# Performance work log

Hardware: AMD Instinct MI355X
Metric: run time of the kernel (lower is better)

The kernel has to match this reference:

```python
import jax, jax.numpy as jnp
import numpy as np

NUM_HEADS = 12
LN_EPS = 1e-5


def _pe(seq_len, d_model):
    # sinusoidal positional encoding buffer (constant)
    pos = np.arange(seq_len, dtype=np.float32)[:, None]
    div = np.exp(np.arange(0, d_model, 2, dtype=np.float32) * (-np.log(10000.0) / d_model))
    pe = np.zeros((seq_len, d_model), dtype=np.float32)
    pe[:, 0::2] = np.sin(pos * div)
    pe[:, 1::2] = np.cos(pos * div)
    return jnp.asarray(pe)


def _ln(x, g, b):
    m = jnp.mean(x, axis=-1, keepdims=True)
    v = jnp.mean(jnp.square(x - m), axis=-1, keepdims=True)
    return (x - m) * jax.lax.rsqrt(v + LN_EPS) * g + b


def setup_inputs() -> dict:
    key = jax.random.key(0)
    B, S, V, D, L, F = 8, 512, 32000, 768, 4, 3072
    ks = jax.random.split(key, 8)
    sc = 0.02
    return {
        "x_ids": jax.random.randint(ks[0], (B, S), 0, V),
        "emb": jax.random.normal(ks[1], (V, D), jnp.float32) * sc,
        "Wq": jax.random.normal(ks[2], (L, D, D), jnp.float32) * sc,
        "bq": jnp.zeros((L, D), jnp.float32),
        "Wk": jax.random.normal(ks[3], (L, D, D), jnp.float32) * sc,
        "bk": jnp.zeros((L, D), jnp.float32),
        "Wv": jax.random.normal(ks[4], (L, D, D), jnp.float32) * sc,
        "bv": jnp.zeros((L, D), jnp.float32),
        "Wo": jax.random.normal(ks[5], (L, D, D), jnp.float32) * sc,
        "bo": jnp.zeros((L, D), jnp.float32),
        "g1": jnp.ones((L, D), jnp.float32),
        "bn1": jnp.zeros((L, D), jnp.float32),
        "W1": jax.random.normal(ks[6], (L, D, F), jnp.float32) * sc,
        "bw1": jnp.zeros((L, F), jnp.float32),
        "W2": jax.random.normal(ks[7], (L, F, D), jnp.float32) * sc,
        "bw2": jnp.zeros((L, D), jnp.float32),
        "g2": jnp.ones((L, D), jnp.float32),
        "bn2": jnp.zeros((L, D), jnp.float32),
    }


def reference(x_ids, emb, Wq, bq, Wk, bk, Wv, bv, Wo, bo, g1, bn1, W1, bw1, W2, bw2, g2, bn2):
    B, S = x_ids.shape
    D = emb.shape[1]
    H = NUM_HEADS
    dk = D // H
    h = emb[x_ids] + _pe(S, D)  # [B,S,D]; dropout is identity (eval)

    def layer(h, p):
        wq, bq_, wk, bk_, wv, bv_, wo, bo_, g1_, bn1_, w1, b1_, w2, b2_, g2_, bn2_ = p

        def heads(y):  # [B,S,D] -> [B,H,S,dk]
            return y.reshape(B, S, H, dk).transpose(0, 2, 1, 3)

        q = heads(h @ wq + bq_)
        k = heads(h @ wk + bk_)
        v = heads(h @ wv + bv_)
        scores = jnp.einsum('bhqd,bhkd->bhqk', q, k) / jnp.sqrt(jnp.float32(dk))
        attn = jax.nn.softmax(scores, axis=-1)
        o = jnp.einsum('bhqk,bhkd->bhqd', attn, v)
        o = o.transpose(0, 2, 1, 3).reshape(B, S, D)
        h = _ln(h + o @ wo + bo_, g1_, bn1_)
        ff = jax.nn.relu(h @ w1 + b1_) @ w2 + b2_
        h = _ln(h + ff, g2_, bn2_)
        return h, None

    h, _ = jax.lax.scan(layer, h, (Wq, bq, Wk, bk, Wv, bv, Wo, bo, g1, bn1, W1, bw1, W2, bw2, g2, bn2))
    return h
```

## Files before the change

kernel.cpp:

```cpp
#include <hip/hip_runtime.h>
#include <stdint.h>

#define B_ 8
#define S_ 512
#define D_ 768
#define H_ 12
#define DK_ 64
#define F_ 3072
#define L_ 4
#define NT_ (B_*S_)
#define BH_ (B_*H_)
#define DQKV_ 2304

typedef __bf16 bf16x8 __attribute__((ext_vector_type(8)));
typedef float f32x4 __attribute__((ext_vector_type(4)));
typedef unsigned short u16x8 __attribute__((ext_vector_type(8)));

static __device__ __forceinline__ unsigned short f2b(float f){
  union { float f; unsigned u; } x; x.f = f;
  unsigned r = x.u + 0x7fffu + ((x.u >> 16) & 1u);
  return (unsigned short)(r >> 16);
}

static __device__ __forceinline__ void gload16(const void* g, void* l){
  __builtin_amdgcn_global_load_lds((const __attribute__((address_space(1))) void*)g,
                                   (__attribute__((address_space(3))) void*)l, 16, 0, 0);
}

static __device__ __forceinline__ float wsum(float v){
  #pragma unroll
  for (int off = 32; off; off >>= 1) v += __shfl_xor(v, off);
  return v;
}

__global__ void wconv_kernel(const float* __restrict__ in, unsigned short* __restrict__ out,
                             int Rr, int Cc, size_t outLS, int rowBase){
  __shared__ float tile[32][33];
  const int l = blockIdx.z;
  in  += (size_t)l*Rr*Cc;
  out += (size_t)l*outLS;
  const int c0 = blockIdx.x*32, r0 = blockIdx.y*32;
  const int tx = threadIdx.x, ty = threadIdx.y;
  #pragma unroll
  for (int i = 0; i < 4; ++i)
    tile[ty+8*i][tx] = in[(size_t)(r0+ty+8*i)*Cc + c0+tx];
  __syncthreads();
  #pragma unroll
  for (int i = 0; i < 4; ++i)
    out[(size_t)(rowBase + c0+ty+8*i)*Rr + r0+tx] = f2b(tile[tx][ty+8*i]);
}

__global__ void bcat_kernel(const float* __restrict__ bq, const float* __restrict__ bk,
                            const float* __restrict__ bv, float* __restrict__ out){
  int i = blockIdx.x*256 + threadIdx.x;
  if (i >= L_*DQKV_) return;
  int l = i / DQKV_, c = i % DQKV_;
  float v = (c < D_) ? bq[l*D_ + c] : (c < 2*D_) ? bk[l*D_ + c - D_] : bv[l*D_ + c - 2*D_];
  out[i] = v;
}

__global__ __launch_bounds__(256) void pe_kernel(float* __restrict__ pe){
  int u = blockIdx.x*256 + threadIdx.x;
  if (u >= S_*384) return;
  int dp = u % 384, s = u / 384;
  int d0 = dp*2;
  float div = __expf((float)d0 * (-9.210340371976184f / 768.0f));
  float ang = (float)s * div;
  pe[(size_t)s*D_ + d0]     = sinf(ang);
  pe[(size_t)s*D_ + d0 + 1] = cosf(ang);
}

__global__ __launch_bounds__(256) void embed_kernel(const int* __restrict__ ids,
                                                    const float* __restrict__ emb,
                                                    const float* __restrict__ pe,
                                                    float* __restrict__ h,
                                                    unsigned short* __restrict__ hb){
  int u = blockIdx.x*256 + threadIdx.x;
  if (u >= NT_*192) return;
  int c = u % 192, t = u / 192, s = t % S_;
  int id = ids[t];
  float4 e = reinterpret_cast<const float4*>(emb + (size_t)id*D_)[c];
  float4 p = reinterpret_cast<const float4*>(pe  + (size_t)s*D_)[c];
  float4 r; r.x = e.x+p.x; r.y = e.y+p.y; r.z = e.z+p.z; r.w = e.w+p.w;
  reinterpret_cast<float4*>(h + (size_t)t*D_)[c] = r;
  ushort4 ub; ub.x = f2b(r.x); ub.y = f2b(r.y); ub.z = f2b(r.z); ub.w = f2b(r.w);
  reinterpret_cast<ushort4*>(hb + (size_t)t*D_)[c] = ub;
}

template<int TN, int KS, bool BIAS, bool RES, bool RELU, bool OUTB>
__global__ __launch_bounds__(256)
void gemm_kernel(const unsigned short* __restrict__ A,
                 const unsigned short* __restrict__ Bt,
                 const float* __restrict__ bias,
                 const float* __restrict__ resid,
                 void* __restrict__ outp,
                 int M, int N, int K)
{
  constexpr int WN = TN/2;
  constexpr int JF = WN/16;
  constexpr int SLOTS = (128+TN)/64;
  __shared__ __attribute__((aligned(16))) unsigned short As[3][128*32];
  __shared__ __attribute__((aligned(16))) unsigned short Bs[3][TN*32];
  const int tid = threadIdx.x;
  const int w = tid >> 6, l = tid & 63;
  const int wm = w >> 1, wn = w & 1;
  const int c16 = l & 15, g = l >> 4;

  const int nwg = gridDim.x;
  const int cpx = nwg >> 3;
  const int sw  = (blockIdx.x & 7)*cpx + (blockIdx.x >> 3);
  const int nbx = N/TN;
  const int nby = M/128;
  const int bx = sw % nbx;
  const int t2 = sw / nbx;
  const int by = t2 % nby;
  const int ks = t2 / nby;
  const int bm = by*128, bn = bx*TN;
  const int Klen = K / KS;
  const int kBeg = ks*Klen;
  const int nk = Klen >> 5;

  auto stage = [&](int buf, int k0){
    #pragma unroll
    for (int s = 0; s < SLOTS; ++s) {
      const int base = s*4096 + w*1024;
      const int x    = base + l*16;
      if (s < 2) {
        const int row  = x >> 6;
        const int csrc = ((x >> 4) & 3) ^ ((row >> 2) & 3);
        gload16(A + (size_t)(bm+row)*K + k0 + csrc*8, (void*)(As[buf] + base/2));
      } else {
        const int o2   = x - 8192;
        const int row  = o2 >> 6;
        const int csrc = ((o2 >> 4) & 3) ^ ((row >> 2) & 3);
        gload16(Bt + (size_t)(bn+row)*K + k0 + csrc*8, (void*)(Bs[buf] + (base-8192)/2));
      }
    }
  };

  f32x4 acc[4][JF] = {};
  const int cswz = (g ^ (c16 >> 2)) * 8;

  stage(0, kBeg);
  stage(1, kBeg + 32);
  stage(2, kBeg + 64);

  for (int t = 0; t < nk; ++t) {
    const int cur = t % 3;
    const int rem = nk - 1 - t;
    if constexpr (SLOTS == 4) {
      if (rem >= 2)      asm volatile("s_waitcnt vmcnt(8)" ::: "memory");
      else if (rem == 1) asm volatile("s_waitcnt vmcnt(4)" ::: "memory");
      else               asm volatile("s_waitcnt vmcnt(0)" ::: "memory");
    } else {
      if (rem >= 2)      asm volatile("s_waitcnt vmcnt(6)" ::: "memory");
      else if (rem == 1) asm volatile("s_waitcnt vmcnt(3)" ::: "memory");
      else               asm volatile("s_waitcnt vmcnt(0)" ::: "memory");
    }
    __builtin_amdgcn_s_barrier();
    __builtin_amdgcn_sched_barrier(0);

    bf16x8 af[4], bfr[JF];
    #pragma unroll
    for (int i = 0; i < 4; ++i)
      af[i]  = *reinterpret_cast<const bf16x8*>(&As[cur][(wm*64 + i*16 + c16)*32 + cswz]);
    #pragma unroll
    for (int j = 0; j < JF; ++j)
      bfr[j] = *reinterpret_cast<const bf16x8*>(&Bs[cur][(wn*WN + j*16 + c16)*32 + cswz]);
    asm volatile("s_waitcnt lgkmcnt(0)" ::: "memory");
    __builtin_amdgcn_sched_barrier(0);
    __builtin_amdgcn_s_barrier();

    if (t + 3 < nk) stage(cur, kBeg + (t+3)*32);

    __builtin_amdgcn_s_setprio(1);
    #pragma unroll
    for (int i = 0; i < 4; ++i)
      #pragma unroll
      for (int j = 0; j < JF; ++j)
        acc[i][j] = __builtin_amdgcn_mfma_f32_16x16x32_bf16(af[i], bfr[j], acc[i][j], 0, 0, 0);
    __builtin_amdgcn_s_setprio(0);
  }

  float* outF = (float*)outp + (size_t)ks*M*N;
  unsigned short* outB = (unsigned short*)outp;
  #pragma unroll
  for (int i = 0; i < 4; ++i) {
    #pragma unroll
    for (int e = 0; e < 4; ++e) {
      const int row = bm + wm*64 + i*16 + (l>>4)*4 + e;
      #pragma unroll
      for (int j = 0; j < JF; ++j) {
        const int col = bn + wn*WN + j*16 + (l&15);
        float v = acc[i][j][e];
        if constexpr (BIAS) v += bias[col];
        if constexpr (RES)  v += resid[(size_t)row*N + col];
        if constexpr (RELU) v = fmaxf(v, 0.f);
        if constexpr (OUTB) outB[(size_t)row*N + col] = f2b(v);
        else                outF[(size_t)row*N + col] = v;
      }
    }
  }
}

__global__ void vtrans_kernel(const unsigned short* __restrict__ v,
                              unsigned short* __restrict__ vt, int ld){
  __shared__ unsigned short tile[32][33];
  const int z = blockIdx.z; const int b = z / H_, hh = z % H_;
  const int j0 = blockIdx.x*32;
  const int d0 = blockIdx.y*32;
  const int tx = threadIdx.x, ty = threadIdx.y;
  const unsigned short* src = v + (size_t)b*S_*ld + hh*DK_;
  #pragma unroll
  for (int i = 0; i < 4; ++i)
    tile[ty+8*i][tx] = src[(size_t)(j0+ty+8*i)*ld + d0+tx];
  __syncthreads();
  unsigned short* dst = vt + (size_t)z*DK_*S_;
  #pragma unroll
  for (int i = 0; i < 4; ++i)
    dst[(size_t)(d0+ty+8*i)*S_ + j0+tx] = tile[tx][ty+8*i];
}

__global__ __launch_bounds__(256)
void fattn_kernel(const unsigned short* __restrict__ qkv,
                  const unsigned short* __restrict__ vt,
                  unsigned short* __restrict__ o)
{
  __shared__ __attribute__((aligned(16))) unsigned short Plds[4*4096];
  const int tid = threadIdx.x;
  const int w = tid >> 6, l = tid & 63;
  const int g = l >> 4, c16 = l & 15;
  const int z = blockIdx.y; const int b = z / H_, hh = z % H_;
  const int q0 = blockIdx.x*128 + w*32;

  const unsigned short* qp = qkv + (size_t)b*S_*DQKV_ + hh*DK_;
  const unsigned short* kp = qp + D_;
  const unsigned short* vv = vt + (size_t)z*DK_*S_;
  char* pbase = (char*)Plds + w*8192;

  bf16x8 qf[2][2];
  #pragma unroll
  for (int jf = 0; jf < 2; ++jf)
    #pragma unroll
    for (int kc = 0; kc < 2; ++kc)
      qf[jf][kc] = *reinterpret_cast<const bf16x8*>(qp + (size_t)(q0 + jf*16 + c16)*DQKV_ + kc*32 + g*8);

  f32x4 acc_o[2][4] = {};
  float m_run[2] = {-1e30f, -1e30f};
  float l_run[2] = {0.f, 0.f};

  for (int kb = 0; kb < S_/128; ++kb) {
    f32x4 acc_s[8][2] = {};
    #pragma unroll
    for (int kt = 0; kt < 8; ++kt) {
      bf16x8 af0 = *reinterpret_cast<const bf16x8*>(kp + (size_t)(kb*128 + kt*16 + c16)*DQKV_ + 0*32 + g*8);
      bf16x8 af1 = *reinterpret_cast<const bf16x8*>(kp + (size_t)(kb*128 + kt*16 + c16)*DQKV_ + 1*32 + g*8);
      #pragma unroll
      for (int jf = 0; jf < 2; ++jf) {
        acc_s[kt][jf] = __builtin_amdgcn_mfma_f32_16x16x32_bf16(af0, qf[jf][0], acc_s[kt][jf], 0, 0, 0);
        acc_s[kt][jf] = __builtin_amdgcn_mfma_f32_16x16x32_bf16(af1, qf[jf][1], acc_s[kt][jf], 0, 0, 0);
      }
    }
    float fac[2];
    #pragma unroll
    for (int jf = 0; jf < 2; ++jf) {
      float vmax = -1e30f;
      #pragma unroll
      for (int kt = 0; kt < 8; ++kt)
        #pragma unroll
        for (int e = 0; e < 4; ++e) {
          acc_s[kt][jf][e] *= 0.125f;
          vmax = fmaxf(vmax, acc_s[kt][jf][e]);
        }
      vmax = fmaxf(vmax, __shfl_xor(vmax, 16));
      vmax = fmaxf(vmax, __shfl_xor(vmax, 32));
      const float m_new = fmaxf(m_run[jf], vmax);
      fac[jf] = __expf(m_run[jf] - m_new);
      float ps = 0.f;
      #pragma unroll
      for (int kt = 0; kt < 8; ++kt)
        #pragma unroll
        for (int e = 0; e < 4; ++e) {
          float p = __expf(acc_s[kt][jf][e] - m_new);
          acc_s[kt][jf][e] = p;
          ps += p;
        }
      ps += __shfl_xor(ps, 16);
      ps += __shfl_xor(ps, 32);
      l_run[jf] = l_run[jf]*fac[jf] + ps;
      m_run[jf] = m_new;
      const int q = jf*16 + c16;
      #pragma unroll
      for (int kt = 0; kt < 8; ++kt) {
        uint2 val;
        val.x = (unsigned)f2b(acc_s[kt][jf][0]) | ((unsigned)f2b(acc_s[kt][jf][1]) << 16);
        val.y = (unsigned)f2b(acc_s[kt][jf][2]) | ((unsigned)f2b(acc_s[kt][jf][3]) << 16);
        int off = (q*256 + kt*32 + g*8) ^ ((q & 7) << 4);
        *reinterpret_cast<uint2*>(pbase + off) = val;
      }
    }
    #pragma unroll
    for (int jr = 0; jr < 2; ++jr)
      #pragma unroll
      for (int e = 0; e < 4; ++e) {
        const float fr = __shfl(fac[jr], g*4 + e);
        #pragma unroll
        for (int jd = 0; jd < 4; ++jd)
          acc_o[jr][jd][e] *= fr;
      }
    #pragma unroll
    for (int kc = 0; kc < 4; ++kc) {
      bf16x8 pa[2], vfr[4];
      #pragma unroll
      for (int jf = 0; jf < 2; ++jf) {
        const int q = jf*16 + c16;
        int off = (q*256 + kc*64 + g*16) ^ ((q & 7) << 4);
        pa[jf] = *reinterpret_cast<const bf16x8*>(pbase + off);
      }
      #pragma unroll
      for (int jd = 0; jd < 4; ++jd)
        vfr[jd] = *reinterpret_cast<const bf16x8*>(vv + (size_t)(jd*16 + c16)*S_ + kb*128 + kc*32 + g*8);
      #pragma unroll
      for (int jf = 0; jf < 2; ++jf)
        #pragma unroll
        for (int jd = 0; jd < 4; ++jd)
          acc_o[jf][jd] = __builtin_amdgcn_mfma_f32_16x16x32_bf16(pa[jf], vfr[jd], acc_o[jf][jd], 0, 0, 0);
    }
  }

  float invl[2] = {1.f/l_run[0], 1.f/l_run[1]};
  unsigned short* ob = o + (size_t)b*S_*D_ + hh*DK_;
  #pragma unroll
  for (int jr = 0; jr < 2; ++jr)
    #pragma unroll
    for (int e = 0; e < 4; ++e) {
      const float ir = __shfl(invl[jr], g*4 + e);
      const int r = q0 + jr*16 + g*4 + e;
      #pragma unroll
      for (int jd = 0; jd < 4; ++jd)
        ob[(size_t)r*D_ + jd*16 + c16] = f2b(acc_o[jr][jd][e] * ir);
    }
}

template<int NP, bool EXTRA>
__global__ __launch_bounds__(256)
void ln_kernel(const float* __restrict__ x,
               const float* __restrict__ resid, const float* __restrict__ bias2,
               const float* __restrict__ g, const float* __restrict__ bta,
               float* __restrict__ ho, unsigned short* __restrict__ hb)
{
  const int w = threadIdx.x >> 6, l = threadIdx.x & 63;
  const size_t row = (size_t)blockIdx.x*4 + w;
  float4 vx[3]; float s1 = 0.f, s2 = 0.f;
  #pragma unroll
  for (int c = 0; c < 3; ++c) {
    vx[c] = reinterpret_cast<const float4*>(x + row*D_)[l + 64*c];
    #pragma unroll
    for (int p = 1; p < NP; ++p) {
      float4 a = reinterpret_cast<const float4*>(x + (size_t)p*NT_*D_ + row*D_)[l + 64*c];
      vx[c].x += a.x; vx[c].y += a.y; vx[c].z += a.z; vx[c].w += a.w;
    }
    if constexpr (EXTRA) {
      float4 r  = reinterpret_cast<const float4*>(resid + row*D_)[l + 64*c];
      float4 bb = reinterpret_cast<const float4*>(bias2)[l + 64*c];
      vx[c].x += r.x + bb.x; vx[c].y += r.y + bb.y;
      vx[c].z += r.z + bb.z; vx[c].w += r.w + bb.w;
    }
    s1 += vx[c].x + vx[c].y + vx[c].z + vx[c].w;
    s2 += vx[c].x*vx[c].x + vx[c].y*vx[c].y + vx[c].z*vx[c].z + vx[c].w*vx[c].w;
  }
  s1 = wsum(s1); s2 = wsum(s2);
  const float mean = s1 * (1.f/768.f);
  const float var  = s2 * (1.f/768.f) - mean*mean;
  const float rs   = rsqrtf(var + 1e-5f);
  const float4* gp = reinterpret_cast<const float4*>(g);
  const float4* bp = reinterpret_cast<const float4*>(bta);
  float4* hp = reinterpret_cast<float4*>(ho + row*D_);
  #pragma unroll
  for (int c = 0; c < 3; ++c) {
    float4 gg = gp[l + 64*c], bb = bp[l + 64*c];
    float4 r;
    r.x = (vx[c].x - mean)*rs*gg.x + bb.x;
    r.y = (vx[c].y - mean)*rs*gg.y + bb.y;
    r.z = (vx[c].z - mean)*rs*gg.z + bb.z;
    r.w = (vx[c].w - mean)*rs*gg.w + bb.w;
    hp[l + 64*c] = r;
    ushort4 u; u.x = f2b(r.x); u.y = f2b(r.y); u.z = f2b(r.z); u.w = f2b(r.w);
    *reinterpret_cast<ushort4*>(hb + row*D_ + (size_t)(l + 64*c)*4) = u;
  }
}

extern "C" void kernel_launch(void* const* d_in, const int* in_sizes, int n_in,
                              void* d_out, int out_size, void* d_ws, size_t ws_size,
                              hipStream_t stream)
{
  const int*   x_ids = (const int*)  d_in[0];
  const float* emb   = (const float*)d_in[1];
  const float* Wq    = (const float*)d_in[2];
  const float* bq    = (const float*)d_in[3];
  const float* Wk    = (const float*)d_in[4];
  const float* bk    = (const float*)d_in[5];
  const float* Wv    = (const float*)d_in[6];
  const float* bv    = (const float*)d_in[7];
  const float* Wo    = (const float*)d_in[8];
  const float* bo    = (const float*)d_in[9];
  const float* g1    = (const float*)d_in[10];
  const float* bn1   = (const float*)d_in[11];
  const float* W1    = (const float*)d_in[12];
  const float* bw1   = (const float*)d_in[13];
  const float* W2    = (const float*)d_in[14];
  const float* bw2   = (const float*)d_in[15];
  const float* g2    = (const float*)d_in[16];
  const float* bn2   = (const float*)d_in[17];

  char* ws = (char*)d_ws;
  size_t off = 0;
  auto alloc = [&](size_t bytes) -> void* {
    void* p = ws + off; off += (bytes + 255) & ~((size_t)255); return p;
  };
  unsigned short* WqkvT = (unsigned short*)alloc((size_t)L_*DQKV_*D_*2);
  unsigned short* WoT = (unsigned short*)alloc((size_t)L_*D_*D_*2);
  unsigned short* W1T = (unsigned short*)alloc((size_t)L_*D_*F_*2);
  unsigned short* W2T = (unsigned short*)alloc((size_t)L_*D_*F_*2);
  float*          bqkv= (float*)         alloc((size_t)L_*DQKV_*4);
  float*          pe  = (float*)         alloc((size_t)S_*D_*4);
  float*          h   = (float*)         alloc((size_t)NT_*D_*4);
  unsigned short* hb  = (unsigned short*)alloc((size_t)NT_*D_*2);
  unsigned short* qkv = (unsigned short*)alloc((size_t)NT_*DQKV_*2);
  unsigned short* vt  = (unsigned short*)alloc((size_t)BH_*DK_*S_*2);
  unsigned short* attnb = (unsigned short*)alloc((size_t)NT_*D_*2);
  float*          y   = (float*)         alloc((size_t)NT_*D_*4);
  unsigned short* f1b = (unsigned short*)alloc((size_t)NT_*F_*2);
  float*          y2p = (float*)         alloc((size_t)3*NT_*D_*4);
  if (off > ws_size) return;

  wconv_kernel<<<dim3(24,24,L_), dim3(32,8), 0, stream>>>(Wq, WqkvT, D_, D_, (size_t)DQKV_*D_, 0);
  wconv_kernel<<<dim3(24,24,L_), dim3(32,8), 0, stream>>>(Wk, WqkvT, D_, D_, (size_t)DQKV_*D_, D_);
  wconv_kernel<<<dim3(24,24,L_), dim3(32,8), 0, stream>>>(Wv, WqkvT, D_, D_, (size_t)DQKV_*D_, 2*D_);
  wconv_kernel<<<dim3(24,24,L_), dim3(32,8), 0, stream>>>(Wo, WoT, D_, D_, (size_t)D_*D_, 0);
  wconv_kernel<<<dim3(96,24,L_), dim3(32,8), 0, stream>>>(W1, W1T, D_, F_, (size_t)D_*F_, 0);
  wconv_kernel<<<dim3(24,96,L_), dim3(32,8), 0, stream>>>(W2, W2T, F_, D_, (size_t)F_*D_, 0);
  bcat_kernel<<<dim3((L_*DQKV_+255)/256), 256, 0, stream>>>(bq, bk, bv, bqkv);

  pe_kernel<<<dim3(S_*384/256), 256, 0, stream>>>(pe);
  embed_kernel<<<dim3(NT_*192/256), 256, 0, stream>>>(x_ids, emb, pe, h, hb);

  for (int l = 0; l < L_; ++l) {
    const unsigned short* wqkvT = WqkvT + (size_t)l*DQKV_*D_;
    const unsigned short* woT = WoT + (size_t)l*D_*D_;
    const unsigned short* w1T = W1T + (size_t)l*D_*F_;
    const unsigned short* w2T = W2T + (size_t)l*D_*F_;

    gemm_kernel<128,1,true,false,false,true><<<576, 256, 0, stream>>>(
        hb, wqkvT, bqkv + l*DQKV_, nullptr, qkv, NT_, DQKV_, D_);

    vtrans_kernel<<<dim3(16,2,BH_), dim3(32,8), 0, stream>>>(qkv + 2*D_, vt, DQKV_);
    fattn_kernel<<<dim3(S_/128, BH_), 256, 0, stream>>>(qkv, vt, attnb);

    gemm_kernel<64,1,true,true,false,false><<<384, 256, 0, stream>>>(
        attnb, woT, bo + l*D_, h, y, NT_, D_, D_);
    ln_kernel<1,false><<<dim3(NT_/4), 256, 0, stream>>>(y, nullptr, nullptr,
        g1 + l*D_, bn1 + l*D_, h, hb);

    gemm_kernel<128,1,true,false,true,true><<<768, 256, 0, stream>>>(
        hb, w1T, bw1 + l*F_, nullptr, f1b, NT_, F_, D_);
    gemm_kernel<128,3,false,false,false,false><<<576, 256, 0, stream>>>(
        f1b, w2T, nullptr, nullptr, y2p, NT_, D_, F_);

    float* hout = (l == L_-1) ? (float*)d_out : h;
    ln_kernel<3,true><<<dim3(NT_/4), 256, 0, stream>>>(y2p, h, bw2 + l*D_,
        g2 + l*D_, bn2 + l*D_, hout, hb);
  }
}
```

Measured before the change: 732.6 us.

## Keep residual stream and GEMM partials in bf16, reduce FFN2 split-K to two

```diff
diff --git a/kernel.cpp b/kernel.cpp
--- a/kernel.cpp
+++ b/kernel.cpp
@@ -21,6 +21,9 @@
   unsigned r = x.u + 0x7fffu + ((x.u >> 16) & 1u);
   return (unsigned short)(r >> 16);
 }
+static __device__ __forceinline__ float b2f(unsigned short u){
+  union { unsigned u; float f; } x; x.u = ((unsigned)u) << 16; return x.f;
+}
 
 static __device__ __forceinline__ void gload16(const void* g, void* l){
   __builtin_amdgcn_global_load_lds((const __attribute__((address_space(1))) void*)g,
@@ -48,6 +51,25 @@
   #pragma unroll
   for (int i = 0; i < 4; ++i)
     out[(size_t)(rowBase + c0+ty+8*i)*Rr + r0+tx] = f2b(tile[tx][ty+8*i]);
+}
+
+__global__ void wconvqkv_kernel(const float* __restrict__ Wq, const float* __restrict__ Wk,
+                                const float* __restrict__ Wv, unsigned short* __restrict__ out){
+  __shared__ float tile[32][33];
+  const int z = blockIdx.z;
+  const int l = z / 3, which = z % 3;
+  const float* in = (which == 0 ? Wq : which == 1 ? Wk : Wv) + (size_t)l*D_*D_;
+  unsigned short* o = out + (size_t)l*DQKV_*D_;
+  const int rowBase = which*D_;
+  const int c0 = blockIdx.x*32, r0 = blockIdx.y*32;
+  const int tx = threadIdx.x, ty = threadIdx.y;
+  #pragma unroll
+  for (int i = 0; i < 4; ++i)
+    tile[ty+8*i][tx] = in[(size_t)(r0+ty+8*i)*D_ + c0+tx];
+  __syncthreads();
+  #pragma unroll
+  for (int i = 0; i < 4; ++i)
+    o[(size_t)(rowBase + c0+ty+8*i)*D_ + r0+tx] = f2b(tile[tx][ty+8*i]);
 }
 
 __global__ void bcat_kernel(const float* __restrict__ bq, const float* __restrict__ bk,
@@ -73,7 +95,6 @@
 __global__ __launch_bounds__(256) void embed_kernel(const int* __restrict__ ids,
                                                     const float* __restrict__ emb,
                                                     const float* __restrict__ pe,
-                                                    float* __restrict__ h,
                                                     unsigned short* __restrict__ hb){
   int u = blockIdx.x*256 + threadIdx.x;
   if (u >= NT_*192) return;
@@ -81,19 +102,17 @@
   int id = ids[t];
   float4 e = reinterpret_cast<const float4*>(emb + (size_t)id*D_)[c];
   float4 p = reinterpret_cast<const float4*>(pe  + (size_t)s*D_)[c];
-  float4 r; r.x = e.x+p.x; r.y = e.y+p.y; r.z = e.z+p.z; r.w = e.w+p.w;
-  reinterpret_cast<float4*>(h + (size_t)t*D_)[c] = r;
-  ushort4 ub; ub.x = f2b(r.x); ub.y = f2b(r.y); ub.z = f2b(r.z); ub.w = f2b(r.w);
+  ushort4 ub; ub.x = f2b(e.x+p.x); ub.y = f2b(e.y+p.y); ub.z = f2b(e.z+p.z); ub.w = f2b(e.w+p.w);
   reinterpret_cast<ushort4*>(hb + (size_t)t*D_)[c] = ub;
 }
 
-template<int TN, int KS, bool BIAS, bool RES, bool RELU, bool OUTB>
+template<int TN, int KS, bool BIAS, bool RES, bool RELU>
 __global__ __launch_bounds__(256)
 void gemm_kernel(const unsigned short* __restrict__ A,
                  const unsigned short* __restrict__ Bt,
                  const float* __restrict__ bias,
-                 const float* __restrict__ resid,
-                 void* __restrict__ outp,
+                 const unsigned short* __restrict__ residB,
+                 unsigned short* __restrict__ outp,
                  int M, int N, int K)
 {
   constexpr int WN = TN/2;
@@ -182,8 +201,7 @@
     __builtin_amdgcn_s_setprio(0);
   }
 
-  float* outF = (float*)outp + (size_t)ks*M*N;
-  unsigned short* outB = (unsigned short*)outp;
+  unsigned short* outB = outp + (size_t)ks*M*N;
   #pragma unroll
   for (int i = 0; i < 4; ++i) {
     #pragma unroll
@@ -194,10 +212,9 @@
         const int col = bn + wn*WN + j*16 + (l&15);
         float v = acc[i][j][e];
         if constexpr (BIAS) v += bias[col];
-        if constexpr (RES)  v += resid[(size_t)row*N + col];
+        if constexpr (RES)  v += b2f(residB[(size_t)row*N + col]);
         if constexpr (RELU) v = fmaxf(v, 0.f);
-        if constexpr (OUTB) outB[(size_t)row*N + col] = f2b(v);
-        else                outF[(size_t)row*N + col] = v;
+        outB[(size_t)row*N + col] = f2b(v);
       }
     }
   }
@@ -342,32 +359,33 @@
     }
 }
 
-template<int NP, bool EXTRA>
+template<int NP, bool EXTRA, bool WF32>
 __global__ __launch_bounds__(256)
-void ln_kernel(const float* __restrict__ x,
-               const float* __restrict__ resid, const float* __restrict__ bias2,
+void ln_kernel(const unsigned short* __restrict__ xb,
+               const unsigned short* __restrict__ resid, const float* __restrict__ bias2,
                const float* __restrict__ g, const float* __restrict__ bta,
                float* __restrict__ ho, unsigned short* __restrict__ hb)
 {
   const int w = threadIdx.x >> 6, l = threadIdx.x & 63;
   const size_t row = (size_t)blockIdx.x*4 + w;
-  float4 vx[3]; float s1 = 0.f, s2 = 0.f;
+  float vx[3][4]; float s1 = 0.f, s2 = 0.f;
   #pragma unroll
   for (int c = 0; c < 3; ++c) {
-    vx[c] = reinterpret_cast<const float4*>(x + row*D_)[l + 64*c];
+    ushort4 u0 = reinterpret_cast<const ushort4*>(xb + row*D_)[l + 64*c];
+    vx[c][0] = b2f(u0.x); vx[c][1] = b2f(u0.y); vx[c][2] = b2f(u0.z); vx[c][3] = b2f(u0.w);
     #pragma unroll
     for (int p = 1; p < NP; ++p) {
-      float4 a = reinterpret_cast<const float4*>(x + (size_t)p*NT_*D_ + row*D_)[l + 64*c];
-      vx[c].x += a.x; vx[c].y += a.y; vx[c].z += a.z; vx[c].w += a.w;
+      ushort4 up = reinterpret_cast<const ushort4*>(xb + (size_t)p*NT_*D_ + row*D_)[l + 64*c];
+      vx[c][0] += b2f(up.x); vx[c][1] += b2f(up.y); vx[c][2] += b2f(up.z); vx[c][3] += b2f(up.w);
     }
     if constexpr (EXTRA) {
-      float4 r  = reinterpret_cast<const float4*>(resid + row*D_)[l + 64*c];
+      ushort4 ur = reinterpret_cast<const ushort4*>(resid + row*D_)[l + 64*c];
       float4 bb = reinterpret_cast<const float4*>(bias2)[l + 64*c];
-      vx[c].x += r.x + bb.x; vx[c].y += r.y + bb.y;
-      vx[c].z += r.z + bb.z; vx[c].w += r.w + bb.w;
-    }
-    s1 += vx[c].x + vx[c].y + vx[c].z + vx[c].w;
-    s2 += vx[c].x*vx[c].x + vx[c].y*vx[c].y + vx[c].z*vx[c].z + vx[c].w*vx[c].w;
+      vx[c][0] += b2f(ur.x) + bb.x; vx[c][1] += b2f(ur.y) + bb.y;
+      vx[c][2] += b2f(ur.z) + bb.z; vx[c][3] += b2f(ur.w) + bb.w;
+    }
+    #pragma unroll
+    for (int e = 0; e < 4; ++e) { s1 += vx[c][e]; s2 += vx[c][e]*vx[c][e]; }
   }
   s1 = wsum(s1); s2 = wsum(s2);
   const float mean = s1 * (1.f/768.f);
@@ -375,18 +393,19 @@
   const float rs   = rsqrtf(var + 1e-5f);
   const float4* gp = reinterpret_cast<const float4*>(g);
   const float4* bp = reinterpret_cast<const float4*>(bta);
-  float4* hp = reinterpret_cast<float4*>(ho + row*D_);
   #pragma unroll
   for (int c = 0; c < 3; ++c) {
     float4 gg = gp[l + 64*c], bb = bp[l + 64*c];
-    float4 r;
-    r.x = (vx[c].x - mean)*rs*gg.x + bb.x;
-    r.y = (vx[c].y - mean)*rs*gg.y + bb.y;
-    r.z = (vx[c].z - mean)*rs*gg.z + bb.z;
-    r.w = (vx[c].w - mean)*rs*gg.w + bb.w;
-    hp[l + 64*c] = r;
-    ushort4 u; u.x = f2b(r.x); u.y = f2b(r.y); u.z = f2b(r.z); u.w = f2b(r.w);
-    *reinterpret_cast<ushort4*>(hb + row*D_ + (size_t)(l + 64*c)*4) = u;
+    float r0 = (vx[c][0] - mean)*rs*gg.x + bb.x;
+    float r1 = (vx[c][1] - mean)*rs*gg.y + bb.y;
+    float r2 = (vx[c][2] - mean)*rs*gg.z + bb.z;
+    float r3 = (vx[c][3] - mean)*rs*gg.w + bb.w;
+    if constexpr (WF32) {
+      float4 r; r.x = r0; r.y = r1; r.z = r2; r.w = r3;
+      reinterpret_cast<float4*>(ho + row*D_)[l + 64*c] = r;
+    }
+    ushort4 u; u.x = f2b(r0); u.y = f2b(r1); u.z = f2b(r2); u.w = f2b(r3);
+    reinterpret_cast<ushort4*>(hb + row*D_)[l + 64*c] = u;
   }
 }
 
@@ -424,26 +443,23 @@
   unsigned short* W2T = (unsigned short*)alloc((size_t)L_*D_*F_*2);
   float*          bqkv= (float*)         alloc((size_t)L_*DQKV_*4);
   float*          pe  = (float*)         alloc((size_t)S_*D_*4);
-  float*          h   = (float*)         alloc((size_t)NT_*D_*4);
   unsigned short* hb  = (unsigned short*)alloc((size_t)NT_*D_*2);
   unsigned short* qkv = (unsigned short*)alloc((size_t)NT_*DQKV_*2);
   unsigned short* vt  = (unsigned short*)alloc((size_t)BH_*DK_*S_*2);
   unsigned short* attnb = (unsigned short*)alloc((size_t)NT_*D_*2);
-  float*          y   = (float*)         alloc((size_t)NT_*D_*4);
+  unsigned short* yb  = (unsigned short*)alloc((size_t)NT_*D_*2);
   unsigned short* f1b = (unsigned short*)alloc((size_t)NT_*F_*2);
-  float*          y2p = (float*)         alloc((size_t)3*NT_*D_*4);
+  unsigned short* y2pb= (unsigned short*)alloc((size_t)2*NT_*D_*2);
   if (off > ws_size) return;
 
-  wconv_kernel<<<dim3(24,24,L_), dim3(32,8), 0, stream>>>(Wq, WqkvT, D_, D_, (size_t)DQKV_*D_, 0);
-  wconv_kernel<<<dim3(24,24,L_), dim3(32,8), 0, stream>>>(Wk, WqkvT, D_, D_, (size_t)DQKV_*D_, D_);
-  wconv_kernel<<<dim3(24,24,L_), dim3(32,8), 0, stream>>>(Wv, WqkvT, D_, D_, (size_t)DQKV_*D_, 2*D_);
+  wconvqkv_kernel<<<dim3(24,24,L_*3), dim3(32,8), 0, stream>>>(Wq, Wk, Wv, WqkvT);
   wconv_kernel<<<dim3(24,24,L_), dim3(32,8), 0, stream>>>(Wo, WoT, D_, D_, (size_t)D_*D_, 0);
   wconv_kernel<<<dim3(96,24,L_), dim3(32,8), 0, stream>>>(W1, W1T, D_, F_, (size_t)D_*F_, 0);
   wconv_kernel<<<dim3(24,96,L_), dim3(32,8), 0, stream>>>(W2, W2T, F_, D_, (size_t)F_*D_, 0);
   bcat_kernel<<<dim3((L_*DQKV_+255)/256), 256, 0, stream>>>(bq, bk, bv, bqkv);
 
   pe_kernel<<<dim3(S_*384/256), 256, 0, stream>>>(pe);
-  embed_kernel<<<dim3(NT_*192/256), 256, 0, stream>>>(x_ids, emb, pe, h, hb);
+  embed_kernel<<<dim3(NT_*192/256), 256, 0, stream>>>(x_ids, emb, pe, hb);
 
   for (int l = 0; l < L_; ++l) {
     const unsigned short* wqkvT = WqkvT + (size_t)l*DQKV_*D_;
@@ -451,24 +467,27 @@
     const unsigned short* w1T = W1T + (size_t)l*D_*F_;
     const unsigned short* w2T = W2T + (size_t)l*D_*F_;
 
-    gemm_kernel<128,1,true,false,false,true><<<576, 256, 0, stream>>>(
+    gemm_kernel<128,1,true,false,false><<<576, 256, 0, stream>>>(
         hb, wqkvT, bqkv + l*DQKV_, nullptr, qkv, NT_, DQKV_, D_);
 
     vtrans_kernel<<<dim3(16,2,BH_), dim3(32,8), 0, stream>>>(qkv + 2*D_, vt, DQKV_);
     fattn_kernel<<<dim3(S_/128, BH_), 256, 0, stream>>>(qkv, vt, attnb);
 
-    gemm_kernel<64,1,true,true,false,false><<<384, 256, 0, stream>>>(
-        attnb, woT, bo + l*D_, h, y, NT_, D_, D_);
-    ln_kernel<1,false><<<dim3(NT_/4), 256, 0, stream>>>(y, nullptr, nullptr,
-        g1 + l*D_, bn1 + l*D_, h, hb);
-
-    gemm_kernel<128,1,true,false,true,true><<<768, 256, 0, stream>>>(
+    gemm_kernel<64,1,true,true,false><<<384, 256, 0, stream>>>(
+        attnb, woT, bo + l*D_, hb, yb, NT_, D_, D_);
+    ln_kernel<1,false,false><<<dim3(NT_/4), 256, 0, stream>>>(yb, nullptr, nullptr,
+        g1 + l*D_, bn1 + l*D_, nullptr, hb);
+
+    gemm_kernel<128,1,true,false,true><<<768, 256, 0, stream>>>(
         hb, w1T, bw1 + l*F_, nullptr, f1b, NT_, F_, D_);
-    gemm_kernel<128,3,false,false,false,false><<<576, 256, 0, stream>>>(
-        f1b, w2T, nullptr, nullptr, y2p, NT_, D_, F_);
-
-    float* hout = (l == L_-1) ? (float*)d_out : h;
-    ln_kernel<3,true><<<dim3(NT_/4), 256, 0, stream>>>(y2p, h, bw2 + l*D_,
-        g2 + l*D_, bn2 + l*D_, hout, hb);
-  }
-}
+    gemm_kernel<128,2,false,false,false><<<384, 256, 0, stream>>>(
+        f1b, w2T, nullptr, nullptr, y2pb, NT_, D_, F_);
+
+    if (l == L_-1)
+      ln_kernel<2,true,true><<<dim3(NT_/4), 256, 0, stream>>>(y2pb, hb, bw2 + l*D_,
+          g2 + l*D_, bn2 + l*D_, (float*)d_out, hb);
+    else
+      ln_kernel<2,true,false><<<dim3(NT_/4), 256, 0, stream>>>(y2pb, hb, bw2 + l*D_,
+          g2 + l*D_, bn2 + l*D_, nullptr, hb);
+  }
+}
```

Measured after the change: 650.2 us. 1.13x faster.
